# Optimization experiments

Hardware: AMD Instinct MI355X
Metric: run time of the kernel (lower is better)

Reference implementation:

```python
import jax, jax.numpy as jnp
import numpy as np

D_MODEL = 1024
D_STATE = 16
D_CONV = 4
EXPAND = 2
HEADDIM = 64
NGROUPS = 1
D_INNER = EXPAND * D_MODEL            # 2048
NHEADS = D_INNER // HEADDIM           # 32
CONV_DIM = D_INNER + 2 * NGROUPS * D_STATE   # 2080
D_IN_PROJ = 2 * D_INNER + 2 * NGROUPS * D_STATE + NHEADS  # 4160
EPS = 1e-5
BATCH, SEQLEN = 4, 2048


def setup_inputs() -> dict:
    key = jax.random.key(0)
    ks = jax.random.split(key, 8)
    x = jax.random.normal(ks[0], (BATCH, SEQLEN, D_MODEL), jnp.float32)
    W_in = jax.random.normal(ks[1], (D_MODEL, D_IN_PROJ), jnp.float32) * 0.02
    conv_w = jax.random.normal(ks[2], (CONV_DIM, D_CONV), jnp.float32) * 0.2
    conv_b = jnp.zeros((CONV_DIM,), jnp.float32)
    # dt_bias = inverse softplus of dt drawn in [1e-3, 1e-1] (mamba_ssm init)
    dt = jax.random.uniform(ks[3], (NHEADS,), jnp.float32, 0.001, 0.1)
    dt_bias = jnp.log(jnp.expm1(dt))
    A_log = jnp.log(jax.random.uniform(ks[4], (NHEADS,), jnp.float32, 1.0, 16.0))
    D_param = jnp.ones((NHEADS,), jnp.float32)
    norm_w = jnp.ones((D_INNER,), jnp.float32)
    W_out = jax.random.normal(ks[5], (D_INNER, D_MODEL), jnp.float32) * 0.02
    layer_scale = jnp.full((D_MODEL,), 1e-4, jnp.float32)
    return dict(x=x, W_in=W_in, conv_w=conv_w, conv_b=conv_b, dt_bias=dt_bias,
                A_log=A_log, D_param=D_param, norm_w=norm_w, W_out=W_out,
                layer_scale=layer_scale)


def _silu(v):
    return v * jax.nn.sigmoid(v)


def _mamba2(x, W_in, conv_w, conv_b, dt_bias, A_log, D_param, norm_w, W_out):
    b, l, _ = x.shape
    zxbcdt = x @ W_in                                  # (b, l, d_in_proj)
    z = zxbcdt[..., :D_INNER]                          # gate
    xBC = zxbcdt[..., D_INNER:D_INNER + CONV_DIM]
    dt = jax.nn.softplus(zxbcdt[..., D_INNER + CONV_DIM:] + dt_bias)  # (b, l, h)
    # causal depthwise conv1d (kernel D_CONV) + SiLU
    xp = jnp.pad(xBC, ((0, 0), (D_CONV - 1, 0), (0, 0)))
    conv = sum(xp[:, k:k + l, :] * conv_w[:, k] for k in range(D_CONV)) + conv_b
    xBC = _silu(conv)
    xs = xBC[..., :D_INNER].reshape(b, l, NHEADS, HEADDIM)  # (b, l, h, p)
    Bm = xBC[..., D_INNER:D_INNER + D_STATE]                # (b, l, n), ngroups=1
    Cm = xBC[..., D_INNER + D_STATE:]                       # (b, l, n)
    A = -jnp.exp(A_log)                                     # (h,)
    dA = jnp.exp(dt * A)                                    # (b, l, h)
    dtx = dt[..., None] * xs                                # (b, l, h, p)

    def step(h, inp):
        dA_t, dtx_t, B_t, C_t = inp
        # h: (b, h, p, n)
        h = h * dA_t[..., None, None] + dtx_t[..., None] * B_t[:, None, None, :]
        y = jnp.einsum('bhpn,bn->bhp', h, C_t)
        return h, y

    h0 = jnp.zeros((b, NHEADS, HEADDIM, D_STATE), x.dtype)
    _, ys = jax.lax.scan(step, h0, (dA.transpose(1, 0, 2), dtx.transpose(1, 0, 2, 3),
                                    Bm.transpose(1, 0, 2), Cm.transpose(1, 0, 2)))
    y = ys.transpose(1, 0, 2, 3) + D_param[None, None, :, None] * xs  # (b, l, h, p)
    y = y.reshape(b, l, D_INNER)
    # gated RMSNorm (norm_before_gate=False): gate first, then rmsnorm
    y = y * _silu(z)
    y = y * jax.lax.rsqrt(jnp.mean(y * y, axis=-1, keepdims=True) + EPS) * norm_w
    return y @ W_out


def reference(x, W_in, conv_w, conv_b, dt_bias, A_log, D_param, norm_w, W_out, layer_scale):
    # dropout is identity (eval / p=0)
    return x + _mamba2(x, W_in, conv_w, conv_b, dt_bias, A_log, D_param, norm_w, W_out) * layer_scale
```

## Files before the change

### kernel.cpp

```cpp
#include <hip/hip_runtime.h>
#include <hip/hip_bf16.h>

#define D_MODEL   1024
#define D_STATE   16
#define D_CONV    4
#define HEADDIM   64
#define NHEADS    32
#define D_INNER   2048
#define CONV_DIM  2080
#define D_IN_PROJ 4160
#define NPAD      4224
#define BATCH     4
#define SEQLEN    2048
#define MROWS     (BATCH*SEQLEN)
#define QCHUNK    64
#define NCHUNK    (SEQLEN/QCHUNK)
#define DT_COL    (2*D_INNER + 2*D_STATE)

#define WSCALE    16.f
#define YSCALE    64.f

__device__ __forceinline__ unsigned short f2b(float f) {
    union { float f; unsigned int u; } v; v.f = f;
    unsigned int r = (v.u + 0x7FFFu + ((v.u >> 16) & 1u)) >> 16;
    return (unsigned short)r;
}
__device__ __forceinline__ float b2f(unsigned short h) {
    union { unsigned int u; float f; } v; v.u = ((unsigned int)h) << 16;
    return v.f;
}
__device__ __forceinline__ unsigned char f2fp8(float f) {
    return (unsigned char)(__builtin_amdgcn_cvt_pk_fp8_f32(f, 0.f, 0, false) & 0xFF);
}

typedef __attribute__((ext_vector_type(8))) short bf16x8;
typedef __attribute__((ext_vector_type(4))) float f32x4;
typedef __attribute__((ext_vector_type(4))) int   i32x4;
typedef __attribute__((ext_vector_type(8))) int   i32x8;

__device__ __forceinline__ i32x8 cat8(i32x4 a, i32x4 b) {
    i32x8 r;
    r[0] = a[0]; r[1] = a[1]; r[2] = a[2]; r[3] = a[3];
    r[4] = b[0]; r[5] = b[1]; r[6] = b[2]; r[7] = b[3];
    return r;
}

__device__ __forceinline__ void async_copy16b(const unsigned char* g, unsigned char* l) {
    __builtin_amdgcn_global_load_lds(
        (const __attribute__((address_space(1))) void*)g,
        (__attribute__((address_space(3))) void*)l, 16, 0, 0);
}

__global__ void cast_f32_fp8(const float* __restrict__ in, unsigned char* __restrict__ out, int n) {
    int i = (blockIdx.x * blockDim.x + threadIdx.x) * 4;
    if (i >= n) return;
    float4 v = *(const float4*)&in[i];
    int p = __builtin_amdgcn_cvt_pk_fp8_f32(v.x, v.y, 0, false);
    p = __builtin_amdgcn_cvt_pk_fp8_f32(v.z, v.w, p, true);
    *(unsigned int*)&out[i] = (unsigned int)p;
}

__global__ void transpose_both(const float* __restrict__ W_in, unsigned char* __restrict__ winT,
                               const float* __restrict__ W_out, unsigned char* __restrict__ woutT,
                               const float* __restrict__ norm_w) {
    __shared__ float tile[64][65];
    int bid = blockIdx.x;
    const float* W; unsigned char* WT; const float* kscale;
    int K, N, bx, by;
    if (bid < 1056) { W = W_in;  WT = winT;  kscale = nullptr; K = 1024; N = 4160; bx = bid % 66; by = bid / 66; }
    else { bid -= 1056; W = W_out; WT = woutT; kscale = norm_w; K = 2048; N = 1024; bx = bid % 16; by = bid / 16; }
    int n0 = bx * 64, k0 = by * 64;
    int tx = threadIdx.x & 63, ty = threadIdx.x >> 6;
    #pragma unroll
    for (int i = 0; i < 16; i++) {
        int r = ty * 16 + i;
        int n = n0 + tx;
        float v = (n < N) ? W[(size_t)(k0 + r) * N + n] : 0.f;
        tile[r][tx] = v;
    }
    __syncthreads();
    float ks = WSCALE * (kscale ? kscale[k0 + tx] : 1.f);
    #pragma unroll
    for (int i = 0; i < 16; i++) {
        int r = ty * 16 + i;
        WT[(size_t)(n0 + r) * K + k0 + tx] = f2fp8(tile[tx][r] * ks);
    }
}

template <int EPI>
__global__ __launch_bounds__(256)
void gemm_fp8(const unsigned char* __restrict__ A, const unsigned char* __restrict__ B,
              int K, int N, unsigned short* __restrict__ Cb,
              float* __restrict__ Cf, const float* __restrict__ xres,
              const float* __restrict__ ls, const float* __restrict__ rs) {
    __shared__ unsigned char lds_a[128 * 128];
    __shared__ unsigned char lds_b[128 * 128];
    const int tid  = threadIdx.x;
    const int wave = tid >> 6;
    const int lane = tid & 63;
    const int bid = blockIdx.x;
    const int xcd = bid & 7, g = bid >> 3;
    const int bm = xcd * 8 + (g & 7);
    const int bn = g >> 3;
    const int wm = wave >> 1, wn = wave & 1;

    f32x4 acc[4][4];
    #pragma unroll
    for (int i = 0; i < 4; i++)
        #pragma unroll
        for (int j = 0; j < 4; j++) acc[i][j] = (f32x4){0.f, 0.f, 0.f, 0.f};

    const int srow = lane >> 3;
    const int sseg = (lane & 7) ^ srow;
    const unsigned char* gA0 = A + (size_t)(bm * 128 + wave * 8 + srow) * K + sseg * 16;
    const unsigned char* gB0 = B + (size_t)(bn * 128 + wave * 8 + srow) * K + sseg * 16;
    const int ldsbase = wave * 8 * 128;

    const int lm = lane & 15, q = lane >> 4;

    for (int k0 = 0; k0 < K; k0 += 128) {
        #pragma unroll
        for (int j = 0; j < 4; j++) {
            async_copy16b(gA0 + k0 + (size_t)(j * 32) * K, &lds_a[ldsbase + j * 32 * 128]);
            async_copy16b(gB0 + k0 + (size_t)(j * 32) * K, &lds_b[ldsbase + j * 32 * 128]);
        }
        __syncthreads();

        i32x8 af[4], bfr[4];
        #pragma unroll
        for (int i = 0; i < 4; i++) {
            int r = wm * 64 + i * 16 + lm;
            int s0 = ((2 * q) ^ (r & 7)) * 16, s1 = ((2 * q + 1) ^ (r & 7)) * 16;
            af[i] = cat8(*(const i32x4*)&lds_a[r * 128 + s0],
                         *(const i32x4*)&lds_a[r * 128 + s1]);
        }
        #pragma unroll
        for (int j = 0; j < 4; j++) {
            int r = wn * 64 + j * 16 + lm;
            int s0 = ((2 * q) ^ (r & 7)) * 16, s1 = ((2 * q + 1) ^ (r & 7)) * 16;
            bfr[j] = cat8(*(const i32x4*)&lds_b[r * 128 + s0],
                          *(const i32x4*)&lds_b[r * 128 + s1]);
        }
        #pragma unroll
        for (int i = 0; i < 4; i++)
            #pragma unroll
            for (int j = 0; j < 4; j++)
                acc[i][j] = __builtin_amdgcn_mfma_scale_f32_16x16x128_f8f6f4(
                    af[i], bfr[j], acc[i][j], 0, 0,
                    0, 0x7F7F7F7F, 0, 0x7F7F7F7F);
        __syncthreads();
    }

    const int row0 = bm * 128 + wm * 64;
    const int col0 = bn * 128 + wn * 64;
    const int lq = (lane >> 4) * 4;
    #pragma unroll
    for (int i = 0; i < 4; i++) {
        #pragma unroll
        for (int j = 0; j < 4; j++) {
            #pragma unroll
            for (int r = 0; r < 4; r++) {
                int gr = row0 + i * 16 + lq + r;
                int gc = col0 + j * 16 + lm;
                float v = acc[i][j][r];
                if (EPI == 0) {
                    Cb[(size_t)gr * N + gc] = f2b(v * (1.f / WSCALE));
                } else {
                    size_t idx = (size_t)gr * 1024 + gc;
                    Cf[idx] = xres[idx] + v * ls[gc] * rs[gr] * (1.f / (WSCALE * YSCALE));
                }
            }
        }
    }
}

__global__ __launch_bounds__(256)
void ssd_hcomp(const unsigned short* __restrict__ zx, const float* __restrict__ dt_bias,
               const float* __restrict__ conv_w, const float* __restrict__ conv_b,
               const float* __restrict__ A_log,
               float* __restrict__ hbuf, float* __restrict__ pbuf,
               unsigned short* __restrict__ xTg, unsigned short* __restrict__ bcg,
               float* __restrict__ scA) {
    __shared__ unsigned short sXraw[67 * 64];
    __shared__ unsigned short sBCraw[67 * 32];
    __shared__ unsigned short sXT[64 * 72];
    __shared__ unsigned short sBC[64 * 32];
    __shared__ unsigned short sBwT[16 * 72];
    __shared__ float sdt[64], scd[64];

    const int blk = blockIdx.x;
    const int c  = blk & 31;
    const int h  = (blk >> 5) & 31;
    const int b  = blk >> 10;
    const int bh = blk >> 5;
    const int row0 = b * SEQLEN + c * QCHUNK;
    const int batch0 = b * SEQLEN;

    const int t    = threadIdx.x;
    const int w    = t >> 6;
    const int lane = t & 63;
    const int lm   = lane & 15;
    const int lq8  = (lane >> 4) * 8;
    const int lq4  = (lane >> 4) * 4;
    const float Ah = -__expf(A_log[h]);

    for (int i = t; i < 536; i += 256) {
        int r = i >> 3, seg = i & 7;
        int gr = row0 - 3 + r;
        int4 v = (gr >= batch0) ? *(const int4*)&zx[(size_t)gr * NPAD + D_INNER + h * 64 + seg * 8]
                                : (int4){0, 0, 0, 0};
        *(int4*)&sXraw[r * 64 + seg * 8] = v;
    }
    for (int i = t; i < 268; i += 256) {
        int r = i >> 2, seg = i & 3;
        int gr = row0 - 3 + r;
        int4 v = (gr >= batch0) ? *(const int4*)&zx[(size_t)gr * NPAD + 2 * D_INNER + seg * 8]
                                : (int4){0, 0, 0, 0};
        *(int4*)&sBCraw[r * 32 + seg * 8] = v;
    }
    if (t < 64) {
        float raw = b2f(zx[(size_t)(row0 + t) * NPAD + DT_COL + h]) + dt_bias[h];
        float dtv = (raw > 20.f) ? raw : log1pf(__expf(raw));
        float v = dtv;
        #pragma unroll
        for (int o = 1; o < 64; o <<= 1) {
            float u = __shfl_up(v, o, 64);
            if (t >= o) v += u;
        }
        sdt[t] = dtv;
        scd[t] = v;
        float sc = __expf(Ah * v);
        float* scrow = &scA[(size_t)(bh * NCHUNK + c) * 192];
        scrow[t] = dtv; scrow[64 + t] = v; scrow[128 + t] = sc;
        if (t == 63) pbuf[bh * NCHUNK + c] = sc;
    }
    __syncthreads();

    {
        const int p = t & 63, sblk = (t >> 6) * 16;
        const int ch = h * 64 + p;
        const float4 cw = *(const float4*)&conv_w[ch * 4];
        const float cb = conv_b[ch];
        float x0 = b2f(sXraw[(sblk + 0) * 64 + p]);
        float x1 = b2f(sXraw[(sblk + 1) * 64 + p]);
        float x2 = b2f(sXraw[(sblk + 2) * 64 + p]);
        #pragma unroll
        for (int i = 0; i < 16; i++) {
            float x3 = b2f(sXraw[(sblk + i + 3) * 64 + p]);
            float acc = cb + cw.x * x0 + cw.y * x1 + cw.z * x2 + cw.w * x3;
            float sv = acc / (1.f + __expf(-acc));
            sXT[p * 72 + sblk + i] = f2b(sv);
            x0 = x1; x1 = x2; x2 = x3;
        }
    }
    {
        const int ch32 = t & 31, s0 = (t >> 5) * 8;
        const int ch = D_INNER + ch32;
        const float4 cw = *(const float4*)&conv_w[ch * 4];
        const float cb = conv_b[ch];
        const float cdl = scd[63];
        float x0 = b2f(sBCraw[(s0 + 0) * 32 + ch32]);
        float x1 = b2f(sBCraw[(s0 + 1) * 32 + ch32]);
        float x2 = b2f(sBCraw[(s0 + 2) * 32 + ch32]);
        #pragma unroll
        for (int i = 0; i < 8; i++) {
            int s = s0 + i;
            float x3 = b2f(sBCraw[(s + 3) * 32 + ch32]);
            float acc = cb + cw.x * x0 + cw.y * x1 + cw.z * x2 + cw.w * x3;
            float sv = acc / (1.f + __expf(-acc));
            sBC[s * 32 + ch32] = f2b(sv);
            if (ch32 < 16) {
                float wgt = sdt[s] * __expf(Ah * (cdl - scd[s]));
                sBwT[ch32 * 72 + s] = f2b(sv * wgt);
            }
            x0 = x1; x1 = x2; x2 = x3;
        }
    }
    __syncthreads();

    f32x4 hacc = (f32x4){0.f, 0.f, 0.f, 0.f};
    #pragma unroll
    for (int ks = 0; ks < 2; ks++) {
        bf16x8 af = *(const bf16x8*)&sBwT[lm * 72 + ks * 32 + lq8];
        bf16x8 bf_ = *(const bf16x8*)&sXT[(w * 16 + lm) * 72 + ks * 32 + lq8];
        hacc = __builtin_amdgcn_mfma_f32_16x16x32_bf16(af, bf_, hacc, 0, 0, 0);
    }
    #pragma unroll
    for (int r = 0; r < 4; r++)
        hbuf[(size_t)(bh * NCHUNK + c) * 1024 + (lq4 + r) * 64 + (w * 16 + lm)] = hacc[r];

    #pragma unroll
    for (int it = 0; it < 2; it++) {
        int idx = t + it * 256;
        int p = idx >> 3, seg = idx & 7;
        *(int4*)&xTg[(size_t)(bh * 64 + p) * SEQLEN + c * 64 + seg * 8] =
            *(const int4*)&sXT[p * 72 + seg * 8];
    }
    if (h == 0) {
        int s = t >> 2, seg = t & 3;
        *(int4*)&bcg[(size_t)(b * SEQLEN + c * 64 + s) * 32 + seg * 8] =
            *(const int4*)&sBC[s * 32 + seg * 8];
    }
}

__global__ __launch_bounds__(1024)
void ssd_state_scan(float* __restrict__ hbuf, const float* __restrict__ pbuf) {
    int bh = blockIdx.x;
    int t = threadIdx.x;
    __shared__ float sP[NCHUNK];
    if (t < NCHUNK) sP[t] = pbuf[bh * NCHUNK + t];
    __syncthreads();
    size_t base = (size_t)bh * NCHUNK * 1024 + t;
    float v[NCHUNK];
    #pragma unroll
    for (int c = 0; c < NCHUNK; c++) v[c] = hbuf[base + (size_t)c * 1024];
    float carry = 0.f;
    #pragma unroll
    for (int c = 0; c < NCHUNK; c++) {
        float tmp = v[c];
        v[c] = carry;
        carry = tmp + sP[c] * carry;
    }
    #pragma unroll
    for (int c = 0; c < NCHUNK; c++) hbuf[base + (size_t)c * 1024] = v[c];
}

__global__ __launch_bounds__(256)
void ssd_yfused(const unsigned short* __restrict__ zx,
                const unsigned short* __restrict__ xTg, const unsigned short* __restrict__ bcg,
                const float* __restrict__ scA,
                const float* __restrict__ A_log, const float* __restrict__ D_param,
                const float* __restrict__ hbuf,
                unsigned char* __restrict__ y, float* __restrict__ ssq) {
    __shared__ unsigned short sXT[64 * 72];
    __shared__ unsigned short sM[64 * 72];
    __shared__ unsigned short sB[64 * 32];
    __shared__ unsigned short sC[64 * 32];
    __shared__ unsigned short sZ[64 * 64];
    __shared__ unsigned short sHT[64 * 40];
    __shared__ float sdt[64], scd[64], sSc[64];

    const int blk = blockIdx.x;
    const int c  = blk & 31;
    const int h  = (blk >> 5) & 31;
    const int b  = blk >> 10;
    const int bh = blk >> 5;
    const int row0 = b * SEQLEN + c * QCHUNK;

    const int t    = threadIdx.x;
    const int w    = t >> 6;
    const int lane = t & 63;
    const int lm   = lane & 15;
    const int lq8  = (lane >> 4) * 8;
    const int lq4  = (lane >> 4) * 4;
    const float Ah = -__expf(A_log[h]);

    #pragma unroll
    for (int it = 0; it < 2; it++) {
        int idx = t + it * 256;
        int p = idx >> 3, seg = idx & 7;
        *(int4*)&sXT[p * 72 + seg * 8] =
            *(const int4*)&xTg[(size_t)(bh * 64 + p) * SEQLEN + c * 64 + seg * 8];
    }
    #pragma unroll
    for (int it = 0; it < 2; it++) {
        int idx = t + it * 256;
        int s = idx >> 3, seg = idx & 7;
        *(int4*)&sZ[s * 64 + seg * 8] =
            *(const int4*)&zx[(size_t)(row0 + s) * NPAD + h * 64 + seg * 8];
    }
    {
        int s = t >> 2, seg = t & 3;
        int4 v = *(const int4*)&bcg[(size_t)(b * SEQLEN + c * 64 + s) * 32 + seg * 8];
        if (seg < 2) *(int4*)&sB[s * 32 + seg * 8] = v;
        else         *(int4*)&sC[s * 32 + (seg - 2) * 8] = v;
    }
    {
        size_t hb = (size_t)(bh * NCHUNK + c) * 1024 + (size_t)t * 4;
        float4 hv = *(const float4*)&hbuf[hb];
        int n = t >> 4;
        int p0 = (t * 4) & 63;
        sHT[(p0 + 0) * 40 + n] = f2b(hv.x);
        sHT[(p0 + 1) * 40 + n] = f2b(hv.y);
        sHT[(p0 + 2) * 40 + n] = f2b(hv.z);
        sHT[(p0 + 3) * 40 + n] = f2b(hv.w);
    }
    if (t < 64) {
        *(int4*)&sB[t * 32 + 16] = (int4){0, 0, 0, 0};
        *(int4*)&sB[t * 32 + 24] = (int4){0, 0, 0, 0};
        *(int4*)&sC[t * 32 + 16] = (int4){0, 0, 0, 0};
        *(int4*)&sC[t * 32 + 24] = (int4){0, 0, 0, 0};
        *(int4*)&sHT[t * 40 + 16] = (int4){0, 0, 0, 0};
        *(int4*)&sHT[t * 40 + 24] = (int4){0, 0, 0, 0};
    }
    if (t < 192) {
        float v = scA[(size_t)(bh * NCHUNK + c) * 192 + t];
        if (t < 64) sdt[t] = v;
        else if (t < 128) scd[t - 64] = v;
        else sSc[t - 128] = v;
    }
    __syncthreads();

    f32x4 sacc[4];
    {
        bf16x8 cfrag = *(const bf16x8*)&sC[(w * 16 + lm) * 32 + lq8];
        #pragma unroll
        for (int sb = 0; sb < 4; sb++) {
            if (sb <= w) {
                bf16x8 bfrag = *(const bf16x8*)&sB[(sb * 16 + lm) * 32 + lq8];
                sacc[sb] = __builtin_amdgcn_mfma_f32_16x16x32_bf16(
                    cfrag, bfrag, (f32x4){0.f, 0.f, 0.f, 0.f}, 0, 0, 0);
            }
        }
    }
    const float Dh = D_param[h];
    #pragma unroll
    for (int sb = 0; sb < 4; sb++) {
        int sp = sb * 16 + lm;
        if (sb > w) {
            #pragma unroll
            for (int r = 0; r < 4; r++) sM[(w * 16 + lq4 + r) * 72 + sp] = 0;
        } else {
            float dts = sdt[sp], cds = scd[sp];
            #pragma unroll
            for (int r = 0; r < 4; r++) {
                int tp = w * 16 + lq4 + r;
                float m = 0.f;
                if (sb < w || sp <= tp) {
                    m = sacc[sb][r] * dts * __expf(Ah * (scd[tp] - cds));
                    if (sp == tp) m += Dh;
                }
                sM[tp * 72 + sp] = f2b(m);
            }
        }
    }

    f32x4 yacc[4];
    #pragma unroll
    for (int pb = 0; pb < 4; pb++) yacc[pb] = (f32x4){0.f, 0.f, 0.f, 0.f};
    #pragma unroll
    for (int ks = 0; ks < 2; ks++) {
        if (ks == 1 && w < 2) continue;
        bf16x8 af = *(const bf16x8*)&sM[(w * 16 + lm) * 72 + ks * 32 + lq8];
        #pragma unroll
        for (int pb = 0; pb < 4; pb++) {
            bf16x8 bf_ = *(const bf16x8*)&sXT[(pb * 16 + lm) * 72 + ks * 32 + lq8];
            yacc[pb] = __builtin_amdgcn_mfma_f32_16x16x32_bf16(af, bf_, yacc[pb], 0, 0, 0);
        }
    }
    f32x4 acc2[4];
    {
        bf16x8 cf2 = *(const bf16x8*)&sC[(w * 16 + lm) * 32 + lq8];
        #pragma unroll
        for (int pb = 0; pb < 4; pb++) {
            bf16x8 hf = *(const bf16x8*)&sHT[(pb * 16 + lm) * 40 + lq8];
            acc2[pb] = __builtin_amdgcn_mfma_f32_16x16x32_bf16(
                cf2, hf, (f32x4){0.f, 0.f, 0.f, 0.f}, 0, 0, 0);
        }
    }

    #pragma unroll
    for (int r = 0; r < 4; r++) {
        const int tp = w * 16 + lq4 + r;
        const size_t yrow = (size_t)(row0 + tp) * D_INNER + h * 64;
        float ssr = 0.f;
        #pragma unroll
        for (int pb = 0; pb < 4; pb++) {
            int pp = pb * 16 + lm;
            float val = yacc[pb][r] + sSc[tp] * acc2[pb][r];
            float zv = b2f(sZ[tp * 64 + pp]);
            float yg = val * (zv / (1.f + __expf(-zv)));
            ssr += yg * yg;
            y[yrow + pp] = f2fp8(yg * YSCALE);
        }
        ssr += __shfl_xor(ssr, 1, 16);
        ssr += __shfl_xor(ssr, 2, 16);
        ssr += __shfl_xor(ssr, 4, 16);
        ssr += __shfl_xor(ssr, 8, 16);
        if (lm == 0)
            ssq[(size_t)(row0 + tp) * NHEADS + h] = ssr;
    }
}

__global__ __launch_bounds__(256)
void rowscale_kernel(const float* __restrict__ ssq, float* __restrict__ rs) {
    int row = blockIdx.x * 256 + threadIdx.x;
    const float4* p = (const float4*)&ssq[(size_t)row * NHEADS];
    float s = 0.f;
    #pragma unroll
    for (int i = 0; i < 8; i++) {
        float4 v = p[i];
        s += v.x + v.y + v.z + v.w;
    }
    rs[row] = rsqrtf(s * (1.f / D_INNER) + 1e-5f);
}

extern "C" void kernel_launch(void* const* d_in, const int* in_sizes, int n_in,
                              void* d_out, int out_size, void* d_ws, size_t ws_size,
                              hipStream_t stream) {
    const float* x        = (const float*)d_in[0];
    const float* W_in     = (const float*)d_in[1];
    const float* conv_w   = (const float*)d_in[2];
    const float* conv_b   = (const float*)d_in[3];
    const float* dt_bias  = (const float*)d_in[4];
    const float* A_log    = (const float*)d_in[5];
    const float* D_param  = (const float*)d_in[6];
    const float* norm_w   = (const float*)d_in[7];
    const float* W_out    = (const float*)d_in[8];
    const float* ls       = (const float*)d_in[9];
    float* out = (float*)d_out;

    char* ws = (char*)d_ws;
    size_t off = 0;
    unsigned char*  x_f8  = (unsigned char*)(ws + off);  off += (size_t)MROWS * D_MODEL;
    unsigned char*  winT  = (unsigned char*)(ws + off);  off += (size_t)NPAD * D_MODEL;
    unsigned char*  woutT = (unsigned char*)(ws + off);  off += (size_t)D_MODEL * D_INNER;
    unsigned short* zx    = (unsigned short*)(ws + off); off += (size_t)MROWS * NPAD * 2;
    float*          pbuf  = (float*)(ws + off);          off += (size_t)BATCH * NHEADS * NCHUNK * 4;
    unsigned char*  yb    = (unsigned char*)(ws + off);  off += (size_t)MROWS * D_INNER;
    float*          ssq   = (float*)(ws + off);          off += (size_t)MROWS * NHEADS * 4;
    float*          rsb   = (float*)(ws + off);          off += (size_t)MROWS * 4;
    float*          hbuf  = (float*)(ws + off);          off += (size_t)BATCH * NHEADS * NCHUNK * 1024 * 4;
    unsigned short* xTg   = (unsigned short*)(ws + off); off += (size_t)MROWS * D_INNER * 2;
    unsigned short* bcg   = (unsigned short*)(ws + off); off += (size_t)MROWS * 32 * 2;
    float*          scA   = (float*)(ws + off);          off += (size_t)BATCH * NHEADS * NCHUNK * 192 * 4;

    cast_f32_fp8<<<(MROWS * D_MODEL) / 1024, 256, 0, stream>>>(x, x_f8, MROWS * D_MODEL);
    transpose_both<<<1568, 256, 0, stream>>>(W_in, winT, W_out, woutT, norm_w);
    gemm_fp8<0><<<(NPAD / 128) * 64, 256, 0, stream>>>(
        x_f8, winT, D_MODEL, NPAD, zx, nullptr, nullptr, nullptr, nullptr);
    ssd_hcomp<<<BATCH * NHEADS * NCHUNK, 256, 0, stream>>>(
        zx, dt_bias, conv_w, conv_b, A_log, hbuf, pbuf, xTg, bcg, scA);
    ssd_state_scan<<<BATCH * NHEADS, 1024, 0, stream>>>(hbuf, pbuf);
    ssd_yfused<<<BATCH * NHEADS * NCHUNK, 256, 0, stream>>>(
        zx, xTg, bcg, scA, A_log, D_param, hbuf, yb, ssq);
    rowscale_kernel<<<MROWS / 256, 256, 0, stream>>>(ssq, rsb);
    gemm_fp8<1><<<(D_MODEL / 128) * 64, 256, 0, stream>>>(
        yb, woutT, D_INNER, D_MODEL, nullptr, out, x, ls, rsb);
}
```

Measured before the change: 262.0 us.

## Merge prep kernels, fold rowscale into out-GEMM, narrow out-GEMM tile, keep z in registers

Combines the fp8 cast of x and the weight transposes into one launch, and computes the RMSNorm row scale inside the output GEMM epilogue, which removes the separate rowscale kernel. The output GEMM now uses 128x64 tiles so it launches twice as many blocks, giving better CU occupancy for the N=1024 problem. ssd_yfused loads the z gate directly into registers instead of staging it through LDS. Together these cut launch count and LDS use. The cost is redundant ssq reductions across the column blocks of the output GEMM and less data reuse per tile.

Result: slower. 269.6 us (+2.9%).

```diff
diff --git a/kernel.cpp b/kernel.cpp
--- a/kernel.cpp
+++ b/kernel.cpp
@@ -51,20 +51,22 @@
         (__attribute__((address_space(3))) void*)l, 16, 0, 0);
 }
 
-__global__ void cast_f32_fp8(const float* __restrict__ in, unsigned char* __restrict__ out, int n) {
-    int i = (blockIdx.x * blockDim.x + threadIdx.x) * 4;
-    if (i >= n) return;
-    float4 v = *(const float4*)&in[i];
-    int p = __builtin_amdgcn_cvt_pk_fp8_f32(v.x, v.y, 0, false);
-    p = __builtin_amdgcn_cvt_pk_fp8_f32(v.z, v.w, p, true);
-    *(unsigned int*)&out[i] = (unsigned int)p;
-}
-
-__global__ void transpose_both(const float* __restrict__ W_in, unsigned char* __restrict__ winT,
-                               const float* __restrict__ W_out, unsigned char* __restrict__ woutT,
-                               const float* __restrict__ norm_w) {
+__global__ __launch_bounds__(256)
+void pre_kernel(const float* __restrict__ x, unsigned char* __restrict__ x_f8,
+                const float* __restrict__ W_in, unsigned char* __restrict__ winT,
+                const float* __restrict__ W_out, unsigned char* __restrict__ woutT,
+                const float* __restrict__ norm_w) {
     __shared__ float tile[64][65];
     int bid = blockIdx.x;
+    if (bid < 8192) {
+        int i = (bid * 256 + threadIdx.x) * 4;
+        float4 v = *(const float4*)&x[i];
+        int p = __builtin_amdgcn_cvt_pk_fp8_f32(v.x, v.y, 0, false);
+        p = __builtin_amdgcn_cvt_pk_fp8_f32(v.z, v.w, p, true);
+        *(unsigned int*)&x_f8[i] = (unsigned int)p;
+        return;
+    }
+    bid -= 8192;
     const float* W; unsigned char* WT; const float* kscale;
     int K, N, bx, by;
     if (bid < 1056) { W = W_in;  WT = winT;  kscale = nullptr; K = 1024; N = 4160; bx = bid % 66; by = bid / 66; }
@@ -87,14 +89,15 @@
     }
 }
 
-template <int EPI>
+template <int EPI, int NF>
 __global__ __launch_bounds__(256)
 void gemm_fp8(const unsigned char* __restrict__ A, const unsigned char* __restrict__ B,
               int K, int N, unsigned short* __restrict__ Cb,
               float* __restrict__ Cf, const float* __restrict__ xres,
-              const float* __restrict__ ls, const float* __restrict__ rs) {
+              const float* __restrict__ ls, const float* __restrict__ ssq) {
+    constexpr int BN = NF * 32;
     __shared__ unsigned char lds_a[128 * 128];
-    __shared__ unsigned char lds_b[128 * 128];
+    __shared__ unsigned char lds_b[BN * 128];
     const int tid  = threadIdx.x;
     const int wave = tid >> 6;
     const int lane = tid & 63;
@@ -104,29 +107,30 @@
     const int bn = g >> 3;
     const int wm = wave >> 1, wn = wave & 1;
 
-    f32x4 acc[4][4];
+    f32x4 acc[4][NF];
     #pragma unroll
     for (int i = 0; i < 4; i++)
         #pragma unroll
-        for (int j = 0; j < 4; j++) acc[i][j] = (f32x4){0.f, 0.f, 0.f, 0.f};
+        for (int j = 0; j < NF; j++) acc[i][j] = (f32x4){0.f, 0.f, 0.f, 0.f};
 
     const int srow = lane >> 3;
     const int sseg = (lane & 7) ^ srow;
     const unsigned char* gA0 = A + (size_t)(bm * 128 + wave * 8 + srow) * K + sseg * 16;
-    const unsigned char* gB0 = B + (size_t)(bn * 128 + wave * 8 + srow) * K + sseg * 16;
+    const unsigned char* gB0 = B + (size_t)(bn * BN  + wave * 8 + srow) * K + sseg * 16;
     const int ldsbase = wave * 8 * 128;
 
     const int lm = lane & 15, q = lane >> 4;
 
     for (int k0 = 0; k0 < K; k0 += 128) {
         #pragma unroll
-        for (int j = 0; j < 4; j++) {
+        for (int j = 0; j < 4; j++)
             async_copy16b(gA0 + k0 + (size_t)(j * 32) * K, &lds_a[ldsbase + j * 32 * 128]);
+        #pragma unroll
+        for (int j = 0; j < NF; j++)
             async_copy16b(gB0 + k0 + (size_t)(j * 32) * K, &lds_b[ldsbase + j * 32 * 128]);
-        }
         __syncthreads();
 
-        i32x8 af[4], bfr[4];
+        i32x8 af[4], bfr[NF];
         #pragma unroll
         for (int i = 0; i < 4; i++) {
             int r = wm * 64 + i * 16 + lm;
@@ -135,8 +139,8 @@
                          *(const i32x4*)&lds_a[r * 128 + s1]);
         }
         #pragma unroll
-        for (int j = 0; j < 4; j++) {
-            int r = wn * 64 + j * 16 + lm;
+        for (int j = 0; j < NF; j++) {
+            int r = wn * (NF * 16) + j * 16 + lm;
             int s0 = ((2 * q) ^ (r & 7)) * 16, s1 = ((2 * q + 1) ^ (r & 7)) * 16;
             bfr[j] = cat8(*(const i32x4*)&lds_b[r * 128 + s0],
                           *(const i32x4*)&lds_b[r * 128 + s1]);
@@ -144,30 +148,46 @@
         #pragma unroll
         for (int i = 0; i < 4; i++)
             #pragma unroll
-            for (int j = 0; j < 4; j++)
+            for (int j = 0; j < NF; j++)
                 acc[i][j] = __builtin_amdgcn_mfma_scale_f32_16x16x128_f8f6f4(
                     af[i], bfr[j], acc[i][j], 0, 0,
                     0, 0x7F7F7F7F, 0, 0x7F7F7F7F);
         __syncthreads();
     }
 
+    float* srs = (float*)lds_a;
+    if constexpr (EPI == 1) {
+        if (tid < 128) {
+            const float4* p = (const float4*)&ssq[(size_t)(bm * 128 + tid) * NHEADS];
+            float s = 0.f;
+            #pragma unroll
+            for (int i2 = 0; i2 < 8; i2++) {
+                float4 v4 = p[i2];
+                s += v4.x + v4.y + v4.z + v4.w;
+            }
+            srs[tid] = rsqrtf(s * (1.f / D_INNER) + 1e-5f);
+        }
+        __syncthreads();
+    }
+
     const int row0 = bm * 128 + wm * 64;
-    const int col0 = bn * 128 + wn * 64;
+    const int col0 = bn * BN + wn * (NF * 16);
     const int lq = (lane >> 4) * 4;
     #pragma unroll
     for (int i = 0; i < 4; i++) {
         #pragma unroll
-        for (int j = 0; j < 4; j++) {
+        for (int j = 0; j < NF; j++) {
             #pragma unroll
             for (int r = 0; r < 4; r++) {
                 int gr = row0 + i * 16 + lq + r;
                 int gc = col0 + j * 16 + lm;
                 float v = acc[i][j][r];
-                if (EPI == 0) {
+                if constexpr (EPI == 0) {
                     Cb[(size_t)gr * N + gc] = f2b(v * (1.f / WSCALE));
                 } else {
                     size_t idx = (size_t)gr * 1024 + gc;
-                    Cf[idx] = xres[idx] + v * ls[gc] * rs[gr] * (1.f / (WSCALE * YSCALE));
+                    float rsv = srs[wm * 64 + i * 16 + lq + r];
+                    Cf[idx] = xres[idx] + v * ls[gc] * rsv * (1.f / (WSCALE * YSCALE));
                 }
             }
         }
@@ -336,7 +356,6 @@
     __shared__ unsigned short sM[64 * 72];
     __shared__ unsigned short sB[64 * 32];
     __shared__ unsigned short sC[64 * 32];
-    __shared__ unsigned short sZ[64 * 64];
     __shared__ unsigned short sHT[64 * 40];
     __shared__ float sdt[64], scd[64], sSc[64];
 
@@ -355,19 +374,19 @@
     const int lq4  = (lane >> 4) * 4;
     const float Ah = -__expf(A_log[h]);
 
+    unsigned short zreg[4][4];
+    #pragma unroll
+    for (int r = 0; r < 4; r++)
+        #pragma unroll
+        for (int pb = 0; pb < 4; pb++)
+            zreg[r][pb] = zx[(size_t)(row0 + w * 16 + lq4 + r) * NPAD + h * 64 + pb * 16 + lm];
+
     #pragma unroll
     for (int it = 0; it < 2; it++) {
         int idx = t + it * 256;
         int p = idx >> 3, seg = idx & 7;
         *(int4*)&sXT[p * 72 + seg * 8] =
             *(const int4*)&xTg[(size_t)(bh * 64 + p) * SEQLEN + c * 64 + seg * 8];
-    }
-    #pragma unroll
-    for (int it = 0; it < 2; it++) {
-        int idx = t + it * 256;
-        int s = idx >> 3, seg = idx & 7;
-        *(int4*)&sZ[s * 64 + seg * 8] =
-            *(const int4*)&zx[(size_t)(row0 + s) * NPAD + h * 64 + seg * 8];
     }
     {
         int s = t >> 2, seg = t & 3;
@@ -468,7 +487,7 @@
         for (int pb = 0; pb < 4; pb++) {
             int pp = pb * 16 + lm;
             float val = yacc[pb][r] + sSc[tp] * acc2[pb][r];
-            float zv = b2f(sZ[tp * 64 + pp]);
+            float zv = b2f(zreg[r][pb]);
             float yg = val * (zv / (1.f + __expf(-zv)));
             ssr += yg * yg;
             y[yrow + pp] = f2fp8(yg * YSCALE);
@@ -480,19 +499,6 @@
         if (lm == 0)
             ssq[(size_t)(row0 + tp) * NHEADS + h] = ssr;
     }
-}
-
-__global__ __launch_bounds__(256)
-void rowscale_kernel(const float* __restrict__ ssq, float* __restrict__ rs) {
-    int row = blockIdx.x * 256 + threadIdx.x;
-    const float4* p = (const float4*)&ssq[(size_t)row * NHEADS];
-    float s = 0.f;
-    #pragma unroll
-    for (int i = 0; i < 8; i++) {
-        float4 v = p[i];
-        s += v.x + v.y + v.z + v.w;
-    }
-    rs[row] = rsqrtf(s * (1.f / D_INNER) + 1e-5f);
 }
 
 extern "C" void kernel_launch(void* const* d_in, const int* in_sizes, int n_in,
@@ -519,22 +525,19 @@
     float*          pbuf  = (float*)(ws + off);          off += (size_t)BATCH * NHEADS * NCHUNK * 4;
     unsigned char*  yb    = (unsigned char*)(ws + off);  off += (size_t)MROWS * D_INNER;
     float*          ssq   = (float*)(ws + off);          off += (size_t)MROWS * NHEADS * 4;
-    float*          rsb   = (float*)(ws + off);          off += (size_t)MROWS * 4;
     float*          hbuf  = (float*)(ws + off);          off += (size_t)BATCH * NHEADS * NCHUNK * 1024 * 4;
     unsigned short* xTg   = (unsigned short*)(ws + off); off += (size_t)MROWS * D_INNER * 2;
     unsigned short* bcg   = (unsigned short*)(ws + off); off += (size_t)MROWS * 32 * 2;
     float*          scA   = (float*)(ws + off);          off += (size_t)BATCH * NHEADS * NCHUNK * 192 * 4;
 
-    cast_f32_fp8<<<(MROWS * D_MODEL) / 1024, 256, 0, stream>>>(x, x_f8, MROWS * D_MODEL);
-    transpose_both<<<1568, 256, 0, stream>>>(W_in, winT, W_out, woutT, norm_w);
-    gemm_fp8<0><<<(NPAD / 128) * 64, 256, 0, stream>>>(
+    pre_kernel<<<8192 + 1568, 256, 0, stream>>>(x, x_f8, W_in, winT, W_out, woutT, norm_w);
+    gemm_fp8<0, 4><<<(NPAD / 128) * 64, 256, 0, stream>>>(
         x_f8, winT, D_MODEL, NPAD, zx, nullptr, nullptr, nullptr, nullptr);
     ssd_hcomp<<<BATCH * NHEADS * NCHUNK, 256, 0, stream>>>(
         zx, dt_bias, conv_w, conv_b, A_log, hbuf, pbuf, xTg, bcg, scA);
     ssd_state_scan<<<BATCH * NHEADS, 1024, 0, stream>>>(hbuf, pbuf);
     ssd_yfused<<<BATCH * NHEADS * NCHUNK, 256, 0, stream>>>(
         zx, xTg, bcg, scA, A_log, D_param, hbuf, yb, ssq);
-    rowscale_kernel<<<MROWS / 256, 256, 0, stream>>>(ssq, rsb);
-    gemm_fp8<1><<<(D_MODEL / 128) * 64, 256, 0, stream>>>(
-        yb, woutT, D_INNER, D_MODEL, nullptr, out, x, ls, rsb);
-}
+    gemm_fp8<1, 2><<<(D_MODEL / 64) * 64, 256, 0, stream>>>(
+        yb, woutT, D_INNER, D_MODEL, nullptr, out, x, ls, ssq);
+}
```
